# Kernel optimization log

Measured on AMD Instinct MI355X. Metric: run time of the kernel, lower is better.

## Reference

```python
import jax, jax.numpy as jnp
import numpy as np

RADIUS = 8
DIMS = (2, 3)


def box_filter_1d(x, dim, r):
    # cumsum along dim, then sliding-window sum via prefix-sum differences,
    # with zero padding at the edges (mirrors the torch cumsum+cat trick).
    cs = jnp.cumsum(x, axis=dim)
    cs = jnp.swapaxes(cs, dim, 0)
    head = cs[r:2 * r + 1]                       # left edge: partial windows
    mid = cs[2 * r + 1:] - cs[:-2 * r - 1]       # full windows
    tail = cs[-1:] - cs[-2 * r - 1:-r - 1]       # right edge: partial windows
    out = jnp.concatenate([head, mid, tail], axis=0)
    return jnp.swapaxes(out, dim, 0)


def setup_inputs() -> dict:
    key = jax.random.key(0)
    tensor = jax.random.normal(key, (8, 32, 512, 512), dtype=jnp.float32)
    return {"tensor": tensor}


def reference(tensor):
    out = tensor
    for dim in DIMS:  # fixed, small structural loop over filtered axes
        assert out.shape[dim] > 2 * RADIUS
        out = box_filter_1d(out, dim, RADIUS)
    return out
```

## Files before the change

### kernel.cpp

```cpp
#include <hip/hip_runtime.h>

#define RADIUS 8
#define N 512
#define TR 32
#define LSTRIDE 516

__global__ __launch_bounds__(512, 4)
void box_kernel(const float* __restrict__ in, float* __restrict__ out) {
    __shared__ __align__(16) float tile[TR * LSTRIDE];

    const int blk   = blockIdx.x;
    const int img   = blk >> 4;
    const int strip = blk & 15;
    const int r0    = strip * TR;
    const float* __restrict__ ibase = in  + (size_t)img * N * N;
    float* __restrict__       obase = out + (size_t)img * N * N;
    const int t = threadIdx.x;

    {
        const int c = t;
        float x[48];
#pragma unroll
        for (int k = 0; k < 48; ++k) {
            const int row = r0 + k - RADIUS;
            x[k] = (row >= 0 && row < N) ? ibase[(size_t)row * N + c] : 0.0f;
        }
        float vs = 0.0f;
#pragma unroll
        for (int k = 0; k <= 2 * RADIUS; ++k) vs += x[k];
#pragma unroll
        for (int i = 0; i < TR; ++i) {
            tile[i * LSTRIDE + c] = vs;
            if (i + 1 < TR) vs += x[i + 2 * RADIUS + 1] - x[i];
        }
    }
    __syncthreads();

    const int qid  = t & 127;
    const int rgrp = t >> 7;
    const int q0   = qid * 4;
#pragma unroll
    for (int i = 0; i < 8; ++i) {
        const int r = rgrp * 8 + i;
        const float* trow = &tile[r * LSTRIDE];
        float wv[20];
#pragma unroll
        for (int p = 0; p < 5; ++p) {
            const int cs = q0 - 8 + 4 * p;
            float4 vv = (cs >= 0 && cs < N)
                      ? *reinterpret_cast<const float4*>(trow + cs)
                      : make_float4(0.0f, 0.0f, 0.0f, 0.0f);
            wv[4 * p + 0] = vv.x; wv[4 * p + 1] = vv.y;
            wv[4 * p + 2] = vv.z; wv[4 * p + 3] = vv.w;
        }
        float s = 0.0f;
#pragma unroll
        for (int k = 0; k < 17; ++k) s += wv[k];
        const float o0 = s;
        const float o1 = o0 - wv[0] + wv[17];
        const float o2 = o1 - wv[1] + wv[18];
        const float o3 = o2 - wv[2] + wv[19];
        *reinterpret_cast<float4*>(obase + (size_t)(r0 + r) * N + q0) =
            make_float4(o0, o1, o2, o3);
    }
}

extern "C" void kernel_launch(void* const* d_in, const int* in_sizes, int n_in,
                              void* d_out, int out_size, void* d_ws, size_t ws_size,
                              hipStream_t stream) {
    const float* in = (const float*)d_in[0];
    float* out = (float*)d_out;
    dim3 grid(8 * 32 * (N / TR));
    dim3 block(512);
    hipLaunchKernelGGL(box_kernel, grid, block, 0, stream, in, out);
}
```

Before: 108.1 us.

## Process eight row strips per block, reusing vertical halo rows in registers

Each block now covers half an image (256 rows) and loops over eight 32-row strips instead of handling a single strip. The 16 halo rows left over from the previous strip are shifted within registers, so only 32 new rows are loaded per strip, which removes the 50% redundant vertical-halo reads. Loads for the next strip are issued before the horizontal pass of the current strip so they can overlap with it. In exchange the grid shrinks from 4096 to 512 blocks, which lowers parallelism across CUs, and each strip adds an extra barrier.

```diff
diff --git a/kernel.cpp b/kernel.cpp
--- a/kernel.cpp
+++ b/kernel.cpp
@@ -3,6 +3,8 @@
 #define RADIUS 8
 #define N 512
 #define TR 32
+#define HALF 256
+#define NSTRIP (HALF / TR)
 #define LSTRIDE 516
 
 __global__ __launch_bounds__(512, 4)
@@ -10,58 +12,77 @@
     __shared__ __align__(16) float tile[TR * LSTRIDE];
 
     const int blk   = blockIdx.x;
-    const int img   = blk >> 4;
-    const int strip = blk & 15;
-    const int r0    = strip * TR;
+    const int img   = blk >> 1;
+    const int half  = blk & 1;
+    const int rbase = half * HALF;
     const float* __restrict__ ibase = in  + (size_t)img * N * N;
     float* __restrict__       obase = out + (size_t)img * N * N;
     const int t = threadIdx.x;
+    const int c = t;
 
-    {
-        const int c = t;
-        float x[48];
+    float x[48];
 #pragma unroll
-        for (int k = 0; k < 48; ++k) {
-            const int row = r0 + k - RADIUS;
-            x[k] = (row >= 0 && row < N) ? ibase[(size_t)row * N + c] : 0.0f;
-        }
-        float vs = 0.0f;
-#pragma unroll
-        for (int k = 0; k <= 2 * RADIUS; ++k) vs += x[k];
-#pragma unroll
-        for (int i = 0; i < TR; ++i) {
-            tile[i * LSTRIDE + c] = vs;
-            if (i + 1 < TR) vs += x[i + 2 * RADIUS + 1] - x[i];
-        }
+    for (int k = 0; k < 48; ++k) {
+        const int row = rbase + k - RADIUS;
+        x[k] = (row >= 0 && row < N) ? ibase[(size_t)row * N + c] : 0.0f;
     }
-    __syncthreads();
 
     const int qid  = t & 127;
     const int rgrp = t >> 7;
     const int q0   = qid * 4;
+
 #pragma unroll
-    for (int i = 0; i < 8; ++i) {
-        const int r = rgrp * 8 + i;
-        const float* trow = &tile[r * LSTRIDE];
-        float wv[20];
+    for (int s = 0; s < NSTRIP; ++s) {
+        const int r0 = rbase + s * TR;
+
+        {
+            float vs = 0.0f;
 #pragma unroll
-        for (int p = 0; p < 5; ++p) {
-            const int cs = q0 - 8 + 4 * p;
-            float4 vv = (cs >= 0 && cs < N)
-                      ? *reinterpret_cast<const float4*>(trow + cs)
-                      : make_float4(0.0f, 0.0f, 0.0f, 0.0f);
-            wv[4 * p + 0] = vv.x; wv[4 * p + 1] = vv.y;
-            wv[4 * p + 2] = vv.z; wv[4 * p + 3] = vv.w;
+            for (int k = 0; k <= 2 * RADIUS; ++k) vs += x[k];
+#pragma unroll
+            for (int i = 0; i < TR; ++i) {
+                tile[i * LSTRIDE + c] = vs;
+                if (i + 1 < TR) vs += x[i + 2 * RADIUS + 1] - x[i];
+            }
         }
-        float s = 0.0f;
+        __syncthreads();
+
+        if (s + 1 < NSTRIP) {
 #pragma unroll
-        for (int k = 0; k < 17; ++k) s += wv[k];
-        const float o0 = s;
-        const float o1 = o0 - wv[0] + wv[17];
-        const float o2 = o1 - wv[1] + wv[18];
-        const float o3 = o2 - wv[2] + wv[19];
-        *reinterpret_cast<float4*>(obase + (size_t)(r0 + r) * N + q0) =
-            make_float4(o0, o1, o2, o3);
+            for (int k = 0; k < 16; ++k) x[k] = x[32 + k];
+#pragma unroll
+            for (int k = 0; k < 32; ++k) {
+                const int row = r0 + TR + RADIUS + k;
+                x[16 + k] = (row < N) ? ibase[(size_t)row * N + c] : 0.0f;
+            }
+        }
+
+#pragma unroll
+        for (int i = 0; i < 8; ++i) {
+            const int r = rgrp * 8 + i;
+            const float* trow = &tile[r * LSTRIDE];
+            float wv[20];
+#pragma unroll
+            for (int p = 0; p < 5; ++p) {
+                const int cs = q0 - 8 + 4 * p;
+                float4 vv = (cs >= 0 && cs < N)
+                          ? *reinterpret_cast<const float4*>(trow + cs)
+                          : make_float4(0.0f, 0.0f, 0.0f, 0.0f);
+                wv[4 * p + 0] = vv.x; wv[4 * p + 1] = vv.y;
+                wv[4 * p + 2] = vv.z; wv[4 * p + 3] = vv.w;
+            }
+            float sum = 0.0f;
+#pragma unroll
+            for (int k = 0; k < 17; ++k) sum += wv[k];
+            const float o0 = sum;
+            const float o1 = o0 - wv[0] + wv[17];
+            const float o2 = o1 - wv[1] + wv[18];
+            const float o3 = o2 - wv[2] + wv[19];
+            *reinterpret_cast<float4*>(obase + (size_t)(r0 + r) * N + q0) =
+                make_float4(o0, o1, o2, o3);
+        }
+
+        if (s + 1 < NSTRIP) __syncthreads();
     }
 }
 
@@ -70,7 +91,7 @@
                               hipStream_t stream) {
     const float* in = (const float*)d_in[0];
     float* out = (float*)d_out;
-    dim3 grid(8 * 32 * (N / TR));
+    dim3 grid(8 * 32 * (N / HALF));
     dim3 block(512);
     hipLaunchKernelGGL(box_kernel, grid, block, 0, stream, in, out);
 }
```

Result: no change. 109.7 us (+1.5%).
